# Optimization experiments

Measured on AMD Instinct MI355X. Metric: run time of the kernel, lower is better.

Reference implementation:

```python
import jax, jax.numpy as jnp
import numpy as np

B, N, DIM = 2, 2048, 1024
HEADS, DIM_HEAD = 16, 64
INNER = HEADS * DIM_HEAD  # 1024
SCALE = DIM_HEAD ** -0.5
EPS = 1e-5


def setup_inputs() -> dict:
    key = jax.random.key(0)
    k1, k2, k3 = jax.random.split(key, 3)
    x = jax.random.normal(k1, (B, N, DIM), dtype=jnp.float32)
    gamma = jnp.ones((DIM,), dtype=jnp.float32)
    beta = jnp.zeros((DIM,), dtype=jnp.float32)
    w_qkv = jax.random.normal(k2, (DIM, 3 * INNER), dtype=jnp.float32) * (DIM ** -0.5)
    w_out = jax.random.normal(k3, (INNER, DIM), dtype=jnp.float32) * (INNER ** -0.5)
    b_out = jnp.zeros((DIM,), dtype=jnp.float32)
    return {"x": x, "gamma": gamma, "beta": beta,
            "w_qkv": w_qkv, "w_out": w_out, "b_out": b_out}


def _layernorm(x, gamma, beta):
    # biased variance, as in nn.LayerNorm / the triton kernel
    mean = jnp.mean(x, axis=-1, keepdims=True)
    xc = x - mean
    var = jnp.mean(xc * xc, axis=-1, keepdims=True)
    return xc * jax.lax.rsqrt(var + EPS) * gamma + beta


def reference(x, gamma, beta, w_qkv, w_out, b_out):
    x = _layernorm(x, gamma, beta)
    qkv = x @ w_qkv                                   # [b, n, 3*inner]
    q, k, v = jnp.split(qkv, 3, axis=-1)
    def to_heads(t):                                  # [b, n, inner] -> [b, h, n, d]
        return t.reshape(B, N, HEADS, DIM_HEAD).transpose(0, 2, 1, 3)
    q, k, v = map(to_heads, (q, k, v))
    q = q * SCALE
    sim = jnp.einsum('bhid,bhjd->bhij', q, k)         # full [b, h, n, n] scores
    attn = jax.nn.softmax(sim, axis=-1)
    out = jnp.einsum('bhij,bhjd->bhid', attn, v)
    out = out.transpose(0, 2, 1, 3).reshape(B, N, INNER)
    return out @ w_out + b_out
```

## Files before the change

kernel.cpp:

```cpp
#include <hip/hip_runtime.h>
#include <hip/hip_bf16.h>

typedef unsigned short u16;
typedef unsigned int u32;
typedef __attribute__((ext_vector_type(8))) short bf16x8;
typedef __attribute__((ext_vector_type(4))) float f32x4;
typedef __attribute__((ext_vector_type(16))) float f32x16;

#define BATCH 2
#define NSEQ 2048
#define DIM 1024
#define HEADS 16
#define DH 64
#define MTOT (BATCH * NSEQ)
#define QKV_N 3072
#define NT (NSEQ / 64)
#define QSCALE_L2E (0.125f * 1.4426950408889634f)

static __device__ __forceinline__ u16 f2bf(float f) {
    union { float f; u32 u; } v; v.f = f;
    u32 r = v.u + 0x7fffu + ((v.u >> 16) & 1u);
    return (u16)(r >> 16);
}

static __device__ __forceinline__ u32 pk2(float a, float b) {
    union { __hip_bfloat162 h; u32 u; } cv;
    cv.h = __float22bfloat162_rn(float2{a, b});
    return cv.u;
}

typedef __attribute__((address_space(1))) const void GV;
typedef __attribute__((address_space(3))) void LV;
static __device__ __forceinline__ void glds16(const void* g, void* l) {
    __builtin_amdgcn_global_load_lds((GV*)g, (LV*)l, 16, 0, 0);
}

__global__ __launch_bounds__(256) void ln_kernel(const float* __restrict__ x,
                                                 const float* __restrict__ gamma,
                                                 const float* __restrict__ beta,
                                                 u16* __restrict__ out) {
    int row = blockIdx.x;
    int t = threadIdx.x;
    const float4* xr = (const float4*)(x + (size_t)row * DIM);
    float4 v = xr[t];
    float s1 = v.x + v.y + v.z + v.w;
    float s2 = v.x * v.x + v.y * v.y + v.z * v.z + v.w * v.w;
    #pragma unroll
    for (int m = 1; m < 64; m <<= 1) {
        s1 += __shfl_xor(s1, m);
        s2 += __shfl_xor(s2, m);
    }
    __shared__ float r1[4], r2[4];
    int wid = t >> 6, lane = t & 63;
    if (lane == 0) { r1[wid] = s1; r2[wid] = s2; }
    __syncthreads();
    s1 = r1[0] + r1[1] + r1[2] + r1[3];
    s2 = r2[0] + r2[1] + r2[2] + r2[3];
    float mean = s1 * (1.0f / DIM);
    float var = s2 * (1.0f / DIM) - mean * mean;
    float rstd = rsqrtf(var + 1e-5f);
    const float4* gr = (const float4*)gamma;
    const float4* br = (const float4*)beta;
    float4 g = gr[t], b = br[t];
    ushort4 ov;
    ov.x = f2bf((v.x - mean) * rstd * g.x + b.x);
    ov.y = f2bf((v.y - mean) * rstd * g.y + b.y);
    ov.z = f2bf((v.z - mean) * rstd * g.z + b.z);
    ov.w = f2bf((v.w - mean) * rstd * g.w + b.w);
    *(ushort4*)(out + (size_t)row * DIM + t * 4) = ov;
}

__global__ __launch_bounds__(256) void transpose_cast_kernel(const float* __restrict__ in,
                                                             u16* __restrict__ out,
                                                             int R, int C) {
    __shared__ float tile[32][33];
    int bx = blockIdx.x;
    int by = blockIdx.y;
    int t = threadIdx.x;
    int lc = t & 31, lr8 = t >> 5;
    #pragma unroll
    for (int i = 0; i < 4; i++) {
        int rr = lr8 + i * 8;
        tile[rr][lc] = in[(size_t)(by * 32 + rr) * C + bx * 32 + lc];
    }
    __syncthreads();
    #pragma unroll
    for (int i = 0; i < 4; i++) {
        int cc = lr8 + i * 8;
        out[(size_t)(bx * 32 + cc) * R + by * 32 + lc] = f2bf(tile[lc][cc]);
    }
}

template <int MODE, int BM, int BN, int CPX>
__global__ __launch_bounds__(256) void gemm_kernel(const u16* __restrict__ A,
                                                   const u16* __restrict__ Bt,
                                                   int M, int N, int K,
                                                   u16* __restrict__ q_out,
                                                   u16* __restrict__ k_out,
                                                   u16* __restrict__ v_out,
                                                   float* __restrict__ out,
                                                   const float* __restrict__ bias) {
    const int BK = 64;
    const int MI = BM / 32;
    const int NJ = BN / 32;
    __shared__ u16 As[BM * BK];
    __shared__ u16 Bs[BN * BK];
    int bid = blockIdx.x;
    int xcd = bid & 7, c = bid >> 3;
    int bn = xcd * CPX + (c % CPX);
    int bm = c / CPX;
    int t = threadIdx.x;
    int wid = t >> 6, lane = t & 63;
    int l15 = lane & 15, l4 = lane >> 4;
    int wm = (wid >> 1) * (BM / 2), wn = (wid & 1) * (BN / 2);

    f32x4 acc[MI][NJ] = {};

    const u16* Abase = A + (size_t)(bm * BM) * K;
    const u16* Bbase = Bt + (size_t)(bn * BN) * K;
    int lrow = lane >> 3;
    int lcol = (lane & 7) * 8;

    for (int k0 = 0; k0 < K; k0 += BK) {
        __syncthreads();
        #pragma unroll
        for (int i = 0; i < BM / 32; i++) {
            int cc = i * 4 + wid;
            int r = cc * 8 + lrow;
            glds16(Abase + (size_t)r * K + k0 + lcol, &As[cc * 512]);
        }
        #pragma unroll
        for (int i = 0; i < BN / 32; i++) {
            int cc = i * 4 + wid;
            int r = cc * 8 + lrow;
            glds16(Bbase + (size_t)r * K + k0 + lcol, &Bs[cc * 512]);
        }
        __syncthreads();
        #pragma unroll
        for (int kk = 0; kk < BK; kk += 32) {
            bf16x8 af[MI], bf[NJ];
            #pragma unroll
            for (int i = 0; i < MI; i++)
                af[i] = *(const bf16x8*)(&As[(wm + i * 16 + l15) * BK + kk + l4 * 8]);
            #pragma unroll
            for (int j = 0; j < NJ; j++)
                bf[j] = *(const bf16x8*)(&Bs[(wn + j * 16 + l15) * BK + kk + l4 * 8]);
            #pragma unroll
            for (int i = 0; i < MI; i++)
                #pragma unroll
                for (int j = 0; j < NJ; j++)
                    acc[i][j] = __builtin_amdgcn_mfma_f32_16x16x32_bf16(af[i], bf[j], acc[i][j], 0, 0, 0);
        }
    }

    if (MODE == 0) {
        int part = (bn * BN) >> 10;
        #pragma unroll
        for (int i = 0; i < MI; i++) {
            #pragma unroll
            for (int j = 0; j < NJ; j++) {
                int gcol = bn * BN + wn + j * 16 + l15;
                int inner = gcol & 1023;
                int hh = inner >> 6, d = inner & 63;
                int n0 = bm * BM + wm + i * 16 + l4 * 4;
                int b = n0 >> 11, n = n0 & 2047;
                if (part == 2) {
                    ushort4 w;
                    w.x = f2bf(acc[i][j][0]); w.y = f2bf(acc[i][j][1]);
                    w.z = f2bf(acc[i][j][2]); w.w = f2bf(acc[i][j][3]);
                    *(ushort4*)(v_out + (((size_t)(b * HEADS + hh)) * DH + d) * NSEQ + n) = w;
                } else {
                    size_t off = (((size_t)(b * HEADS + hh)) * NSEQ + n) * DH + d;
                    #pragma unroll
                    for (int r = 0; r < 4; r++) {
                        float val = acc[i][j][r];
                        if (part == 0) q_out[off + (size_t)r * DH] = f2bf(val * QSCALE_L2E);
                        else           k_out[off + (size_t)r * DH] = f2bf(val);
                    }
                }
            }
        }
    } else {
        #pragma unroll
        for (int i = 0; i < MI; i++) {
            #pragma unroll
            for (int j = 0; j < NJ; j++) {
                #pragma unroll
                for (int r = 0; r < 4; r++) {
                    int grow = bm * BM + wm + i * 16 + l4 * 4 + r;
                    int gcol = bn * BN + wn + j * 16 + l15;
                    out[(size_t)grow * N + gcol] = acc[i][j][r] + bias[gcol];
                }
            }
        }
    }
}

__global__ __launch_bounds__(256) void attn_kernel(const u16* __restrict__ Q,
                                                   const u16* __restrict__ Kg,
                                                   const u16* __restrict__ VTg,
                                                   u16* __restrict__ out) {
    __shared__ u16 Ks[2][64 * 64];
    __shared__ u16 Vs[2][64 * 64];

    int bid = blockIdx.x;
    int wg = (bid & 7) * 64 + (bid >> 3);
    int qt = wg & 15;
    int bh = wg >> 4;

    const u16* Qh = Q   + (size_t)bh * NSEQ * DH;
    const u16* Kh = Kg  + (size_t)bh * NSEQ * DH;
    const u16* Vh = VTg + (size_t)bh * DH * NSEQ;

    int t = threadIdx.x, wid = t >> 6, lane = t & 63;
    int q = lane & 31, h = lane >> 5;
    int qrow = qt * 128 + wid * 32 + q;

    bf16x8 qf[4];
    #pragma unroll
    for (int kk = 0; kk < 4; kk++)
        qf[kk] = *(const bf16x8*)(Qh + (size_t)qrow * DH + kk * 16 + h * 8);

    f32x16 o0 = {}, o1 = {};
    float ell = 0.f;

    int srow = t >> 2, sc4 = t & 3;
    int cA = (sc4 * 2) ^ (srow & 7);
    int cB = (sc4 * 2 + 1) ^ (srow & 7);
    const u16* kpg = Kh + (size_t)srow * DH + sc4 * 16;
    const u16* vpg = Vh + (size_t)srow * NSEQ + sc4 * 16;
    int swq = q & 7;

#define VPERM(P0, P1, B0, B1)                                                   \
    int4 P0 = make_int4((B0).x, (B0).y, (B1).x, (B1).y);                        \
    int4 P1 = make_int4((B0).z, (B0).w, (B1).z, (B1).w);

#define QK_CLUSTER(S0v, S1v, KSB)                                               \
    do {                                                                        \
        __builtin_amdgcn_s_setprio(1);                                          \
        _Pragma("unroll")                                                       \
        for (int kk = 0; kk < 4; kk++) {                                        \
            int sl = kk * 2 + h;                                                \
            bf16x8 a0 = *(const bf16x8*)(&KSB[q * 64 + ((sl ^ swq) << 3)]);     \
            bf16x8 a1 = *(const bf16x8*)(&KSB[(32 + q) * 64 + ((sl ^ swq) << 3)]); \
            S0v = __builtin_amdgcn_mfma_f32_32x32x16_bf16(a0, qf[kk], S0v, 0, 0, 0); \
            S1v = __builtin_amdgcn_mfma_f32_32x32x16_bf16(a1, qf[kk], S1v, 0, 0, 0); \
        }                                                                       \
        __builtin_amdgcn_s_setprio(0);                                          \
        __builtin_amdgcn_sched_barrier(0);                                      \
    } while (0)

#define SM_PV(S0v, S1v, VSB)                                                    \
    do {                                                                        \
        _Pragma("unroll")                                                       \
        for (int i = 0; i < 16; i++) {                                          \
            S0v[i] = __builtin_amdgcn_exp2f(S0v[i]);                            \
            S1v[i] = __builtin_amdgcn_exp2f(S1v[i]);                            \
        }                                                                       \
        float a8[8];                                                            \
        _Pragma("unroll")                                                       \
        for (int i = 0; i < 8; i++)                                             \
            a8[i] = (S0v[i] + S0v[i + 8]) + (S1v[i] + S1v[i + 8]);              \
        float rs = ((a8[0] + a8[4]) + (a8[1] + a8[5])) + ((a8[2] + a8[6]) + (a8[3] + a8[7])); \
        rs += __shfl_xor(rs, 32);                                               \
        ell += rs;                                                              \
        u32 pk0[4][2], pk1[4][2];                                               \
        _Pragma("unroll")                                                       \
        for (int g = 0; g < 4; g++) {                                           \
            pk0[g][0] = pk2(S0v[4 * g], S0v[4 * g + 1]);                        \
            pk0[g][1] = pk2(S0v[4 * g + 2], S0v[4 * g + 3]);                    \
            pk1[g][0] = pk2(S1v[4 * g], S1v[4 * g + 1]);                        \
            pk1[g][1] = pk2(S1v[4 * g + 2], S1v[4 * g + 3]);                    \
        }                                                                       \
        __builtin_amdgcn_s_setprio(1);                                          \
        _Pragma("unroll")                                                       \
        for (int ks = 0; ks < 4; ks++) {                                        \
            union { u32 w[4]; bf16x8 v; } bb;                                   \
            if (ks == 0)      { bb.w[0] = pk0[0][0]; bb.w[1] = pk0[0][1];       \
                                bb.w[2] = pk0[1][0]; bb.w[3] = pk0[1][1]; }     \
            else if (ks == 1) { bb.w[0] = pk0[2][0]; bb.w[1] = pk0[2][1];       \
                                bb.w[2] = pk0[3][0]; bb.w[3] = pk0[3][1]; }     \
            else if (ks == 2) { bb.w[0] = pk1[0][0]; bb.w[1] = pk1[0][1];       \
                                bb.w[2] = pk1[1][0]; bb.w[3] = pk1[1][1]; }     \
            else              { bb.w[0] = pk1[2][0]; bb.w[1] = pk1[2][1];       \
                                bb.w[2] = pk1[3][0]; bb.w[3] = pk1[3][1]; }     \
            int sl = ks * 2 + h;                                                \
            bf16x8 f0 = *(const bf16x8*)(&VSB[q * 64 + ((sl ^ swq) << 3)]);     \
            bf16x8 f1 = *(const bf16x8*)(&VSB[(32 + q) * 64 + ((sl ^ swq) << 3)]); \
            o0 = __builtin_amdgcn_mfma_f32_32x32x16_bf16(f0, bb.v, o0, 0, 0, 0);\
            o1 = __builtin_amdgcn_mfma_f32_32x32x16_bf16(f1, bb.v, o1, 0, 0, 0);\
        }                                                                       \
        __builtin_amdgcn_s_setprio(0);                                          \
    } while (0)

#define STEP(SC0, SC1, SN0, SN1, I, KS_NEXT, VS_CUR, VS_WR, KS_WR)              \
    do {                                                                        \
        __syncthreads();                                                        \
        if ((I) + 1 < NT) {                                                     \
            SN0 = (f32x16){}; SN1 = (f32x16){};                                 \
            QK_CLUSTER(SN0, SN1, KS_NEXT);                                      \
        }                                                                       \
        int4 nv0, nv1, nk0, nk1;                                                \
        bool ldv = (I) + 1 < NT, ldk = (I) + 2 < NT;                            \
        if (ldv) {                                                              \
            nv0 = *(const int4*)(vpg + ((I) + 1) * 64);                         \
            nv1 = *(const int4*)(vpg + ((I) + 1) * 64 + 8);                     \
        }                                                                       \
        if (ldk) {                                                              \
            nk0 = *(const int4*)(kpg + (size_t)(((I) + 2) * 64) * DH);          \
            nk1 = *(const int4*)(kpg + (size_t)(((I) + 2) * 64) * DH + 8);      \
        }                                                                       \
        SM_PV(SC0, SC1, VS_CUR);                                                \
        if (ldv) {                                                              \
            VPERM(pv0, pv1, nv0, nv1)                                           \
            *(int4*)&VS_WR[srow * 64 + cA * 8] = pv0;                           \
            *(int4*)&VS_WR[srow * 64 + cB * 8] = pv1;                           \
        }                                                                       \
        if (ldk) {                                                              \
            *(int4*)&KS_WR[srow * 64 + cA * 8] = nk0;                           \
            *(int4*)&KS_WR[srow * 64 + cB * 8] = nk1;                           \
        }                                                                       \
    } while (0)

    {
        int4 a0 = *(const int4*)(kpg);
        int4 a1 = *(const int4*)(kpg + 8);
        int4 b0 = *(const int4*)(vpg);
        int4 b1 = *(const int4*)(vpg + 8);
        *(int4*)&Ks[0][srow * 64 + cA * 8] = a0;
        *(int4*)&Ks[0][srow * 64 + cB * 8] = a1;
        VPERM(pb0, pb1, b0, b1)
        *(int4*)&Vs[0][srow * 64 + cA * 8] = pb0;
        *(int4*)&Vs[0][srow * 64 + cB * 8] = pb1;
        a0 = *(const int4*)(kpg + (size_t)64 * DH);
        a1 = *(const int4*)(kpg + (size_t)64 * DH + 8);
        __syncthreads();
        *(int4*)&Ks[1][srow * 64 + cA * 8] = a0;
        *(int4*)&Ks[1][srow * 64 + cB * 8] = a1;
    }
    f32x16 sA0 = {}, sA1 = {}, sB0 = {}, sB1 = {};
    QK_CLUSTER(sA0, sA1, Ks[0]);

    for (int i = 0; i < NT; i += 2) {
        STEP(sA0, sA1, sB0, sB1, i,     Ks[1], Vs[0], Vs[1], Ks[0]);
        STEP(sB0, sB1, sA0, sA1, i + 1, Ks[0], Vs[1], Vs[0], Ks[1]);
    }

#undef STEP
#undef SM_PV
#undef QK_CLUSTER
#undef VPERM

    int b = bh >> 4, hh = bh & 15;
    float rinv = __builtin_amdgcn_rcpf(ell);
    u16* orow = out + ((size_t)(b * NSEQ) + qrow) * DIM + hh * DH;
    #pragma unroll
    for (int rq = 0; rq < 4; rq++) {
        ushort4 w0, w1;
        w0.x = f2bf(o0[4 * rq] * rinv);     w0.y = f2bf(o0[4 * rq + 1] * rinv);
        w0.z = f2bf(o0[4 * rq + 2] * rinv); w0.w = f2bf(o0[4 * rq + 3] * rinv);
        w1.x = f2bf(o1[4 * rq] * rinv);     w1.y = f2bf(o1[4 * rq + 1] * rinv);
        w1.z = f2bf(o1[4 * rq + 2] * rinv); w1.w = f2bf(o1[4 * rq + 3] * rinv);
        int d0 = 8 * rq + 4 * h;
        *(ushort4*)(orow + d0) = w0;
        *(ushort4*)(orow + 32 + d0) = w1;
    }
}

extern "C" void kernel_launch(void* const* d_in, const int* in_sizes, int n_in,
                              void* d_out, int out_size, void* d_ws, size_t ws_size,
                              hipStream_t stream) {
    const float* x     = (const float*)d_in[0];
    const float* gamma = (const float*)d_in[1];
    const float* beta  = (const float*)d_in[2];
    const float* w_qkv = (const float*)d_in[3];
    const float* w_out = (const float*)d_in[4];
    const float* b_out = (const float*)d_in[5];
    float* out = (float*)d_out;

    char* ws = (char*)d_ws;
    u16* x_ln  = (u16*)ws; ws += (size_t)MTOT * DIM * 2;
    u16* wqkvT = (u16*)ws; ws += (size_t)QKV_N * DIM * 2;
    u16* woutT = (u16*)ws; ws += (size_t)DIM * DIM * 2;
    u16* Qb    = (u16*)ws; ws += (size_t)BATCH * HEADS * NSEQ * DH * 2;
    u16* Kb    = (u16*)ws; ws += (size_t)BATCH * HEADS * NSEQ * DH * 2;
    u16* VTb   = (u16*)ws; ws += (size_t)BATCH * HEADS * NSEQ * DH * 2;
    u16* attn  = (u16*)ws; ws += (size_t)MTOT * DIM * 2;

    ln_kernel<<<MTOT, 256, 0, stream>>>(x, gamma, beta, x_ln);
    transpose_cast_kernel<<<dim3(QKV_N / 32, DIM / 32), 256, 0, stream>>>(w_qkv, wqkvT, DIM, QKV_N);
    transpose_cast_kernel<<<dim3(DIM / 32, DIM / 32), 256, 0, stream>>>(w_out, woutT, DIM, DIM);

    gemm_kernel<0, 128, 64, 6><<<1536, 256, 0, stream>>>(
        x_ln, wqkvT, MTOT, QKV_N, DIM, Qb, Kb, VTb, nullptr, nullptr);

    attn_kernel<<<512, 256, 0, stream>>>(Qb, Kb, VTb, attn);

    gemm_kernel<1, 64, 128, 1><<<512, 256, 0, stream>>>(
        attn, woutT, MTOT, DIM, DIM, nullptr, nullptr, nullptr, out, b_out);
}
```

Baseline: 130.1 us.

## Double-buffer GEMM shared-memory tiles to overlap global loads with MFMA

Splits the GEMM's A and B LDS tiles into two buffers. The loads for the next K-slice are issued before computing on the current slice, and the loop now has one barrier per iteration instead of two. The aim is to hide global-to-LDS load latency behind MFMA work. In exchange, shared memory per block doubles, which may reduce occupancy. Correctness depends on the single barrier also covering completion of the async glds loads.

```diff
diff --git a/kernel.cpp b/kernel.cpp
--- a/kernel.cpp
+++ b/kernel.cpp
@@ -103,8 +103,8 @@
     const int BK = 64;
     const int MI = BM / 32;
     const int NJ = BN / 32;
-    __shared__ u16 As[BM * BK];
-    __shared__ u16 Bs[BN * BK];
+    __shared__ u16 As[2][BM * BK];
+    __shared__ u16 Bs[2][BN * BK];
     int bid = blockIdx.x;
     int xcd = bid & 7, c = bid >> 3;
     int bn = xcd * CPX + (c % CPX);
@@ -121,37 +121,49 @@
     int lrow = lane >> 3;
     int lcol = (lane & 7) * 8;
 
+#define GSTAGE(K0, B)                                                           \
+    do {                                                                        \
+        _Pragma("unroll")                                                       \
+        for (int i = 0; i < BM / 32; i++) {                                     \
+            int cc = i * 4 + wid;                                               \
+            int r = cc * 8 + lrow;                                              \
+            glds16(Abase + (size_t)r * K + (K0) + lcol, &As[B][cc * 512]);      \
+        }                                                                       \
+        _Pragma("unroll")                                                       \
+        for (int i = 0; i < BN / 32; i++) {                                     \
+            int cc = i * 4 + wid;                                               \
+            int r = cc * 8 + lrow;                                              \
+            glds16(Bbase + (size_t)r * K + (K0) + lcol, &Bs[B][cc * 512]);      \
+        }                                                                       \
+    } while (0)
+
+    GSTAGE(0, 0);
+    __syncthreads();
+
+    int cur = 0;
     for (int k0 = 0; k0 < K; k0 += BK) {
-        __syncthreads();
-        #pragma unroll
-        for (int i = 0; i < BM / 32; i++) {
-            int cc = i * 4 + wid;
-            int r = cc * 8 + lrow;
-            glds16(Abase + (size_t)r * K + k0 + lcol, &As[cc * 512]);
-        }
-        #pragma unroll
-        for (int i = 0; i < BN / 32; i++) {
-            int cc = i * 4 + wid;
-            int r = cc * 8 + lrow;
-            glds16(Bbase + (size_t)r * K + k0 + lcol, &Bs[cc * 512]);
-        }
-        __syncthreads();
+        if (k0 + BK < K) GSTAGE(k0 + BK, cur ^ 1);
+        const u16* AsC = As[cur];
+        const u16* BsC = Bs[cur];
         #pragma unroll
         for (int kk = 0; kk < BK; kk += 32) {
             bf16x8 af[MI], bf[NJ];
             #pragma unroll
             for (int i = 0; i < MI; i++)
-                af[i] = *(const bf16x8*)(&As[(wm + i * 16 + l15) * BK + kk + l4 * 8]);
+                af[i] = *(const bf16x8*)(&AsC[(wm + i * 16 + l15) * BK + kk + l4 * 8]);
             #pragma unroll
             for (int j = 0; j < NJ; j++)
-                bf[j] = *(const bf16x8*)(&Bs[(wn + j * 16 + l15) * BK + kk + l4 * 8]);
+                bf[j] = *(const bf16x8*)(&BsC[(wn + j * 16 + l15) * BK + kk + l4 * 8]);
             #pragma unroll
             for (int i = 0; i < MI; i++)
                 #pragma unroll
                 for (int j = 0; j < NJ; j++)
                     acc[i][j] = __builtin_amdgcn_mfma_f32_16x16x32_bf16(af[i], bf[j], acc[i][j], 0, 0, 0);
         }
-    }
+        __syncthreads();
+        cur ^= 1;
+    }
+#undef GSTAGE
 
     if (MODE == 0) {
         int part = (bn * BN) >> 10;
```

Result: no change. 130.2 us (median of 2 runs) (+0.1%).
